# Optimization experiments

Measured on AMD Instinct MI355X. Metric: run time of the kernel, lower is better.

## Reference

```python
import jax, jax.numpy as jnp
import numpy as np

IMPOSSIBLE = -10000.0
TAGSET_SIZE = 64
NUM_TAGS = TAGSET_SIZE + 2  # C = 66
START_IDX = NUM_TAGS - 2
STOP_IDX = NUM_TAGS - 1
B, L, D = 32, 1024, 1024


def setup_inputs() -> dict:
    key = jax.random.key(0)
    k1, k2, k3, k4, k5 = jax.random.split(key, 5)
    features = jax.random.normal(k1, (B, L, D), dtype=jnp.float32)
    ys = jax.random.randint(k2, (B, L), 0, TAGSET_SIZE).astype(jnp.int64)
    masks = jnp.ones((B, L), dtype=jnp.float32)
    fc_w = jax.random.normal(k3, (D, NUM_TAGS), dtype=jnp.float32) / np.sqrt(D)
    fc_b = jax.random.normal(k4, (NUM_TAGS,), dtype=jnp.float32) * 0.01
    transitions = jax.random.normal(k5, (NUM_TAGS, NUM_TAGS), dtype=jnp.float32)
    # transitions TO start and FROM stop are impossible (torch indexing [to, from])
    transitions = transitions.at[START_IDX, :].set(IMPOSSIBLE)
    transitions = transitions.at[:, STOP_IDX].set(IMPOSSIBLE)
    return {"features": features, "ys": ys, "masks": masks,
            "fc_w": fc_w, "fc_b": fc_b, "transitions": transitions}


def _forward_algorithm(feats, masks, transitions):
    """CRF partition function. feats: [B,L,C], masks: [B,L] -> [B]."""
    Bb, Ll, C = feats.shape
    scores0 = jnp.full((Bb, C), IMPOSSIBLE, dtype=feats.dtype).at[:, START_IDX].set(0.0)

    def step(scores, xs):
        emit_t, m_t = xs  # emit_t: [B,C], m_t: [B]
        # score_t[b, j] = logsumexp_i( scores[b,i] + trans[j,i] + emit[b,j] )
        score_t = jax.nn.logsumexp(
            scores[:, None, :] + transitions[None, :, :] + emit_t[:, :, None], axis=-1)
        scores = score_t * m_t[:, None] + scores * (1.0 - m_t[:, None])
        return scores, None

    xs = (jnp.swapaxes(feats, 0, 1), jnp.swapaxes(masks, 0, 1))  # [L,B,C], [L,B]
    scores, _ = jax.lax.scan(step, scores0, xs)
    return jax.nn.logsumexp(scores + transitions[STOP_IDX][None, :], axis=-1)


def _score_sentence(feats, tags, masks, transitions):
    """Score of the gold tag path. feats: [B,L,C], tags: [B,L] -> [B]."""
    Bb, Ll, C = feats.shape
    emit = jnp.take_along_axis(feats, tags[:, :, None], axis=2)[:, :, 0]  # [B,L]
    start = jnp.full((Bb, 1), START_IDX, dtype=tags.dtype)
    tags_ext = jnp.concatenate([start, tags], axis=1)  # [B,L+1]
    trans_sc = transitions[tags_ext[:, 1:], tags_ext[:, :-1]]  # [B,L]
    lengths = masks.sum(1).astype(jnp.int32)  # [B]
    last_tag = tags_ext[jnp.arange(Bb), lengths]  # [B]
    last_score = transitions[STOP_IDX, last_tag]
    return ((trans_sc + emit) * masks).sum(1) + last_score


def reference(features, ys, masks, fc_w, fc_b, transitions):
    feats = jnp.einsum('bld,dc->blc', features, fc_w) + fc_b  # [B,L,C]
    masks_ = masks.astype(feats.dtype)
    forward_score = _forward_algorithm(feats, masks_, transitions)  # [B]
    gold_score = _score_sentence(feats, ys.astype(jnp.int32), masks_, transitions)  # [B]
    return (forward_score, gold_score)
```

## Files before the change

kernel.cpp:

```cpp
#include <hip/hip_runtime.h>
#include <hip/hip_bf16.h>
#include <stdint.h>


#define START_IDX 64
#define STOP_IDX 65
#define LN2F 0.6931471805599453f

typedef __attribute__((ext_vector_type(4))) float f32x4;
typedef __attribute__((ext_vector_type(8))) __bf16 bf16x8;
typedef __attribute__((ext_vector_type(4))) __bf16 bf16x4;

__device__ __forceinline__ void gload_lds16(const void* g, void* l) {
  __builtin_amdgcn_global_load_lds(
      (const __attribute__((address_space(1))) void*)g,
      (__attribute__((address_space(3))) void*)l, 16, 0, 0);
}

template <int CTRL>
__device__ __forceinline__ float dpp_mov(float v) {
  return __int_as_float(
      __builtin_amdgcn_update_dpp(0, __float_as_int(v), CTRL, 0xF, 0xF, true));
}
__device__ __forceinline__ float wave_max64(float v) {
  v = fmaxf(v, dpp_mov<0xB1>(v));
  v = fmaxf(v, dpp_mov<0x4E>(v));
  v = fmaxf(v, dpp_mov<0x141>(v));
  v = fmaxf(v, dpp_mov<0x140>(v));
  v = fmaxf(v, dpp_mov<0x142>(v));
  v = fmaxf(v, dpp_mov<0x143>(v));
  return v;
}
__device__ __forceinline__ float wave_sum64(float v) {
  v += dpp_mov<0xB1>(v);
  v += dpp_mov<0x4E>(v);
  v += dpp_mov<0x141>(v);
  v += dpp_mov<0x140>(v);
  v += dpp_mov<0x142>(v);
  v += dpp_mov<0x143>(v);
  return v;
}

__global__ __launch_bounds__(256) void crf_wcvt(const float* __restrict__ W,
                                                unsigned short* __restrict__ Wbt) {
  __shared__ float tile[64][65];
  const int t = threadIdx.x;
  const int kb = blockIdx.x;
#pragma unroll
  for (int i = 0; i < 16; ++i) {
    const int f = i * 256 + t;
    const int k = f >> 6, n = f & 63;
    tile[k][n] = W[(kb * 64 + k) * 66 + n];
  }
  __syncthreads();
#pragma unroll
  for (int i = 0; i < 16; ++i) {
    const int f = i * 256 + t;
    const int n = f >> 6, k = f & 63;
    union { __bf16 h; unsigned short u; } cv;
    cv.h = (__bf16)tile[k][n];
    Wbt[n * 1024 + kb * 64 + k] = cv.u;
  }
}

__global__ __launch_bounds__(256) void crf_fwd(const float* __restrict__ features,
                                               const unsigned short* __restrict__ Wbt,
                                               const float* __restrict__ bias,
                                               const float* __restrict__ masks,
                                               const float* __restrict__ trans,
                                               float* __restrict__ featsOut,
                                               float* __restrict__ chunkP,
                                               int* __restrict__ chunkExp) {
  __shared__ __align__(16) float As[4096];
  __shared__ __align__(16) unsigned short Bs[4096];
  __shared__ __align__(16) float expE[64][64];
  __shared__ __align__(16) unsigned short T[2][4096];
  __shared__ float wmax[2][4];
  const int tid = threadIdx.x;
  const int w = tid >> 6, lane = tid & 63, g = lane >> 4, q = lane & 15;
  const int c = blockIdx.x, b = blockIdx.y;

  {
    f32x4 z4 = {0.f, 0.f, 0.f, 0.f};
    *(f32x4*)((char*)T[0] + tid * 16) = z4;
    *(f32x4*)((char*)T[0] + 4096 + tid * 16) = z4;
    __syncthreads();
    if (tid < 64) {
      const int off = tid * 128 + ((2 * tid) ^ ((tid & 7) << 4));
      *(unsigned short*)((char*)T[0] + off) = (unsigned short)0x3F80;
    }
    if (tid < 4) wmax[0][tid] = 1.0f;
  }

  {
    const float* Abase = features + ((size_t)b << 20) + ((size_t)(c << 6) << 10);
    f32x4 acc[4];
#pragma unroll
    for (int nt = 0; nt < 4; ++nt) acc[nt] = (f32x4){0.f, 0.f, 0.f, 0.f};

    const int sA = (q & 7) << 4;
    for (int k0 = 0; k0 < 1024; k0 += 64) {
#pragma unroll
      for (int j = 0; j < 4; ++j) {
        const int row = 16 * w + 4 * j + (lane >> 4);
        const int colb = ((lane & 15) * 16) ^ ((row & 7) << 4);
        gload_lds16((const char*)(Abase + (size_t)row * 1024 + k0) + colb,
                    (char*)As + (16 * w + 4 * j) * 256);
      }
#pragma unroll
      for (int j = 0; j < 2; ++j) {
        const int n = 16 * w + 8 * j + (lane >> 3);
        const int colb = ((lane & 7) * 16) ^ ((n & 7) << 4);
        gload_lds16((const char*)(Wbt + (size_t)n * 1024 + k0) + colb,
                    (char*)Bs + (16 * w + 8 * j) * 128);
      }
      __syncthreads();
#pragma unroll
      for (int kk = 0; kk < 64; kk += 32) {
        const char* Ab = (const char*)As + (16 * w + q) * 256;
        float4 alo = *(const float4*)(Ab + ((kk * 4 + 32 * g) ^ sA));
        float4 ahi = *(const float4*)(Ab + ((kk * 4 + 32 * g + 16) ^ sA));
        bf16x8 af;
        af[0] = (__bf16)alo.x; af[1] = (__bf16)alo.y;
        af[2] = (__bf16)alo.z; af[3] = (__bf16)alo.w;
        af[4] = (__bf16)ahi.x; af[5] = (__bf16)ahi.y;
        af[6] = (__bf16)ahi.z; af[7] = (__bf16)ahi.w;
#pragma unroll
        for (int nt = 0; nt < 4; ++nt) {
          const int n = q + 16 * nt;
          bf16x8 bf = *(const bf16x8*)((const char*)Bs + n * 128 +
                                       ((kk * 2 + 16 * g) ^ ((n & 7) << 4)));
          acc[nt] = __builtin_amdgcn_mfma_f32_16x16x32_bf16(af, bf, acc[nt], 0, 0, 0);
        }
      }
      __syncthreads();
    }
    const float bb0 = bias[q + 0], bb1 = bias[q + 16];
    const float bb2 = bias[q + 32], bb3 = bias[q + 48];
#pragma unroll
    for (int r = 0; r < 4; ++r) {
      const int tl = 16 * w + 4 * g + r;
      float* orow = featsOut + (((size_t)(b << 10) + (c << 6) + tl) << 6) + q;
      const float v0 = acc[0][r] + bb0, v1 = acc[1][r] + bb1;
      const float v2 = acc[2][r] + bb2, v3 = acc[3][r] + bb3;
      orow[0] = v0; orow[16] = v1; orow[32] = v2; orow[48] = v3;
      expE[tl][q + 0]  = __expf(v0);
      expE[tl][q + 16] = __expf(v1);
      expE[tl][q + 32] = __expf(v2);
      expE[tl][q + 48] = __expf(v3);
    }
  }

  bf16x8 Ea0, Ea1;
  {
    const int i = 16 * w + q;
    const float* tp0 = trans + i * 66 + 8 * g;
    const float* tp1 = tp0 + 32;
#pragma unroll
    for (int e = 0; e < 8; ++e) {
      Ea0[e] = (__bf16)__expf(tp0[e]);
      Ea1[e] = (__bf16)__expf(tp1[e]);
    }
  }

  float pv[4][4];
#pragma unroll
  for (int nt = 0; nt < 4; ++nt)
#pragma unroll
    for (int r = 0; r < 4; ++r)
      pv[nt][r] = ((16 * w + 4 * g + r) == (q + 16 * nt)) ? 1.f : 0.f;

  const int t0 = (c == 0) ? 1 : (c << 6);
  const int t1 = (c << 6) + 64;
  const float* mb = masks + (b << 10);
  const int tml = t0 + lane;
  const float mkv = mb[tml > 1023 ? 1023 : tml];

  int e_acc = 0;
  int cur = 0;
  __syncthreads();

  for (int t = t0; t < t1; ++t) {
    const int tl = t - (c << 6);
    const float4 ee = *(const float4*)&expE[tl][16 * w + 4 * g];
    const float m =
        __int_as_float(__builtin_amdgcn_readlane(__float_as_int(mkv), t - t0));
    if (m != 0.f) {
      const char* Tb = (const char*)T[cur];
      f32x4 acc[4];
#pragma unroll
      for (int nt = 0; nt < 4; ++nt) {
        const int n = q + 16 * nt;
        const int sw = (n & 7) << 4;
        bf16x8 B0 = *(const bf16x8*)(Tb + n * 128 + ((16 * g) ^ sw));
        bf16x8 B1 = *(const bf16x8*)(Tb + n * 128 + ((64 + 16 * g) ^ sw));
        f32x4 z = {0.f, 0.f, 0.f, 0.f};
        z = __builtin_amdgcn_mfma_f32_16x16x32_bf16(Ea0, B0, z, 0, 0, 0);
        acc[nt] = __builtin_amdgcn_mfma_f32_16x16x32_bf16(Ea1, B1, z, 0, 0, 0);
      }
      const float4 wm = *(const float4*)wmax[cur];
      const float mx = fmaxf(fmaxf(wm.x, wm.y), fmaxf(wm.z, wm.w));
      const int ex = ((__float_as_int(mx) >> 23) & 0xFF) - 127;
      const float sc = __int_as_float((127 - ex) << 23);
      float ce[4];
      ce[0] = ee.x * sc; ce[1] = ee.y * sc; ce[2] = ee.z * sc; ce[3] = ee.w * sc;
      float lm = 0.f;
#pragma unroll
      for (int nt = 0; nt < 4; ++nt) {
#pragma unroll
        for (int r = 0; r < 4; ++r) {
          float val = acc[nt][r] * ce[r];
          if (m != 1.f) val = m * val + (1.f - m) * sc * pv[nt][r];
          pv[nt][r] = val;
          lm = fmaxf(lm, val);
        }
      }
      lm = wave_max64(lm);
      const int nxt = cur ^ 1;
      char* Tw = (char*)T[nxt];
#pragma unroll
      for (int nt = 0; nt < 4; ++nt) {
        bf16x4 o;
        o[0] = (__bf16)pv[nt][0]; o[1] = (__bf16)pv[nt][1];
        o[2] = (__bf16)pv[nt][2]; o[3] = (__bf16)pv[nt][3];
        const int n = q + 16 * nt;
        *(bf16x4*)(Tw + n * 128 + ((32 * w + 8 * g) ^ ((n & 7) << 4))) = o;
      }
      if (lane == 63) wmax[nxt][w] = lm;
      e_acc += ex;
      __syncthreads();
      cur = nxt;
    }
  }

#pragma unroll
  for (int nt = 0; nt < 4; ++nt)
#pragma unroll
    for (int r = 0; r < 4; ++r)
      chunkP[(((size_t)(b * 16 + c)) << 12) + (size_t)(16 * w + 4 * g + r) * 64 +
             q + 16 * nt] = pv[nt][r];
  if (tid == 0) chunkExp[b * 16 + c] = e_acc;
}

__global__ void crf_fin(const float* __restrict__ feats,
                        const int* __restrict__ ys,
                        const float* __restrict__ masks,
                        const float* __restrict__ trans,
                        const float* __restrict__ chunkP,
                        const int* __restrict__ chunkExp,
                        float* __restrict__ out) {
  __shared__ __align__(16) float vb[64];
  const int lane = threadIdx.x;
  const int b = blockIdx.x >> 1;
  if ((blockIdx.x & 1) == 0) {
    float v = __expf(feats[((size_t)b << 16) + lane]) *
              __expf(trans[lane * 66 + START_IDX]);
    int e_acc = 0;
    for (int cc = 0; cc < 16; ++cc) {
      vb[lane] = v;
      __builtin_amdgcn_wave_barrier();
      const float* Pr = chunkP + (((size_t)(b * 16 + cc)) << 12) + (size_t)lane * 64;
      float q0 = 0.f, q1 = 0.f, q2 = 0.f, q3 = 0.f;
#pragma unroll
      for (int j4 = 0; j4 < 16; ++j4) {
        float4 p = *(const float4*)(Pr + 4 * j4);
        float4 x = ((const float4*)vb)[j4];
        q0 = fmaf(p.x, x.x, q0); q1 = fmaf(p.y, x.y, q1);
        q2 = fmaf(p.z, x.z, q2); q3 = fmaf(p.w, x.w, q3);
      }
      const float qq = (q0 + q1) + (q2 + q3);
      float mx = wave_max64(qq);
      mx = __int_as_float(__builtin_amdgcn_readlane(__float_as_int(mx), 63));
      const int ex = ((__float_as_int(mx) >> 23) & 0xFF) - 127;
      v = qq * __int_as_float((127 - ex) << 23);
      e_acc += ex + chunkExp[b * 16 + cc];
      __builtin_amdgcn_wave_barrier();
    }
    const float sum = wave_sum64(v * __expf(trans[STOP_IDX * 66 + lane]));
    const float s =
        __int_as_float(__builtin_amdgcn_readlane(__float_as_int(sum), 63));
    if (lane == 0) out[b] = __logf(s) + (float)e_acc * LN2F;
  } else {
    const float* fb = feats + ((size_t)b << 16);
    const float* mb = masks + (b << 10);
    const int* yb = ys + (b << 10);
    float s = 0.f, cnt = 0.f;
#pragma unroll
    for (int cc = 0; cc < 16; ++cc) {
      const int t = cc * 64 + lane;
      const float m = mb[t];
      const int y = yb[t];
      const int yp = (t == 0) ? START_IDX : yb[t - 1];
      s += (trans[y * 66 + yp] + fb[t * 64 + y]) * m;
      cnt += m;
    }
    float tot = wave_sum64(s);
    float len = wave_sum64(cnt);
    int totb = __builtin_amdgcn_readlane(__float_as_int(tot), 63);
    int lenb = __builtin_amdgcn_readlane(__float_as_int(len), 63);
    if (lane == 0) {
      const int Lr = (int)__int_as_float(lenb);
      const int last = (Lr == 0) ? START_IDX : yb[Lr - 1];
      out[32 + b] = __int_as_float(totb) + trans[STOP_IDX * 66 + last];
    }
  }
}

extern "C" void kernel_launch(void* const* d_in, const int* in_sizes, int n_in,
                              void* d_out, int out_size, void* d_ws, size_t ws_size,
                              hipStream_t stream) {
  const float* features = (const float*)d_in[0];
  const int* ys         = (const int*)d_in[1];
  const float* masks    = (const float*)d_in[2];
  const float* fc_w     = (const float*)d_in[3];
  const float* fc_b     = (const float*)d_in[4];
  const float* trans    = (const float*)d_in[5];
  float* outp = (float*)d_out;

  char* ws = (char*)d_ws;
  float* feats_ws = (float*)ws;
  unsigned short* Wbt = (unsigned short*)(ws + 8388608);
  float* chunkP = (float*)(ws + 8388608 + 131072);
  int* chunkExp = (int*)(ws + 8388608 + 131072 + 8388608);

  crf_wcvt<<<16, 256, 0, stream>>>(fc_w, Wbt);
  dim3 cg(16, 32);
  crf_fwd<<<cg, 256, 0, stream>>>(features, Wbt, fc_b, masks, trans,
                                  feats_ws, chunkP, chunkExp);
  crf_fin<<<64, 64, 0, stream>>>(feats_ws, ys, masks, trans, chunkP, chunkExp, outp);
}
```

Measured before the change: 274.8 us.

## Halve CRF chunk length, double-buffer GEMM loads, and reuse shared memory

Sequence chunks shrink from 64 to 32 timesteps, so each sequence gets 32 chunks and the forward kernel launches twice as many blocks. The serial per-chunk matrix-product recurrence becomes shorter, at the cost of a longer final chain in crf_fin and twice the chunkP workspace. The projection GEMM now double-buffers its global-to-LDS loads with one barrier per k-step, and its waves split the 32x64 tile in a 2x2 layout. Shared memory is unified into one 32KB buffer that is reused for expE and the transfer matrices, which may raise occupancy. The wave max reduction is also moved after the bf16 stores.

```diff
diff --git a/kernel.cpp b/kernel.cpp
--- a/kernel.cpp
+++ b/kernel.cpp
@@ -71,84 +71,99 @@
                                                float* __restrict__ featsOut,
                                                float* __restrict__ chunkP,
                                                int* __restrict__ chunkExp) {
-  __shared__ __align__(16) float As[4096];
-  __shared__ __align__(16) unsigned short Bs[4096];
-  __shared__ __align__(16) float expE[64][64];
-  __shared__ __align__(16) unsigned short T[2][4096];
+  __shared__ __align__(16) char smem[32768];
   __shared__ float wmax[2][4];
   const int tid = threadIdx.x;
   const int w = tid >> 6, lane = tid & 63, g = lane >> 4, q = lane & 15;
   const int c = blockIdx.x, b = blockIdx.y;
+  const int rb = w & 1, cb = w >> 1;
+
+  const float* Abase = features + ((size_t)b << 20) + ((size_t)c << 15);
 
   {
-    f32x4 z4 = {0.f, 0.f, 0.f, 0.f};
-    *(f32x4*)((char*)T[0] + tid * 16) = z4;
-    *(f32x4*)((char*)T[0] + 4096 + tid * 16) = z4;
-    __syncthreads();
-    if (tid < 64) {
-      const int off = tid * 128 + ((2 * tid) ^ ((tid & 7) << 4));
-      *(unsigned short*)((char*)T[0] + off) = (unsigned short)0x3F80;
-    }
-    if (tid < 4) wmax[0][tid] = 1.0f;
-  }
-
-  {
-    const float* Abase = features + ((size_t)b << 20) + ((size_t)(c << 6) << 10);
-    f32x4 acc[4];
-#pragma unroll
-    for (int nt = 0; nt < 4; ++nt) acc[nt] = (f32x4){0.f, 0.f, 0.f, 0.f};
+    const int arow0 = 8 * w + (lane >> 4);
+    const int acolb = ((lane & 15) * 16);
+    const int brow0 = 16 * w + (lane >> 3);
+    const int bcolb = ((lane & 7) * 16);
+
+    f32x4 acc[2];
+    acc[0] = (f32x4){0.f, 0.f, 0.f, 0.f};
+    acc[1] = (f32x4){0.f, 0.f, 0.f, 0.f};
+
+#pragma unroll
+    for (int j = 0; j < 2; ++j) {
+      const int row = arow0 + 4 * j;
+      gload_lds16((const char*)(Abase + (size_t)row * 1024) +
+                      (acolb ^ ((row & 7) << 4)),
+                  smem + (8 * w + 4 * j) * 256);
+      const int n = brow0 + 8 * j;
+      gload_lds16((const char*)(Wbt + (size_t)n * 1024) +
+                      (bcolb ^ ((n & 7) << 4)),
+                  smem + 16384 + (16 * w + 8 * j) * 128);
+    }
 
     const int sA = (q & 7) << 4;
-    for (int k0 = 0; k0 < 1024; k0 += 64) {
-#pragma unroll
-      for (int j = 0; j < 4; ++j) {
-        const int row = 16 * w + 4 * j + (lane >> 4);
-        const int colb = ((lane & 15) * 16) ^ ((row & 7) << 4);
-        gload_lds16((const char*)(Abase + (size_t)row * 1024 + k0) + colb,
-                    (char*)As + (16 * w + 4 * j) * 256);
-      }
-#pragma unroll
-      for (int j = 0; j < 2; ++j) {
-        const int n = 16 * w + 8 * j + (lane >> 3);
-        const int colb = ((lane & 7) * 16) ^ ((n & 7) << 4);
-        gload_lds16((const char*)(Wbt + (size_t)n * 1024 + k0) + colb,
-                    (char*)Bs + (16 * w + 8 * j) * 128);
-      }
+    for (int kt = 0; kt < 16; ++kt) {
+      const int buf = kt & 1;
       __syncthreads();
-#pragma unroll
-      for (int kk = 0; kk < 64; kk += 32) {
-        const char* Ab = (const char*)As + (16 * w + q) * 256;
-        float4 alo = *(const float4*)(Ab + ((kk * 4 + 32 * g) ^ sA));
-        float4 ahi = *(const float4*)(Ab + ((kk * 4 + 32 * g + 16) ^ sA));
+      if (kt < 15) {
+        const int k0 = (kt + 1) * 64;
+#pragma unroll
+        for (int j = 0; j < 2; ++j) {
+          const int row = arow0 + 4 * j;
+          gload_lds16((const char*)(Abase + (size_t)row * 1024 + k0) +
+                          (acolb ^ ((row & 7) << 4)),
+                      smem + (buf ^ 1) * 8192 + (8 * w + 4 * j) * 256);
+          const int n = brow0 + 8 * j;
+          gload_lds16((const char*)(Wbt + (size_t)n * 1024 + k0) +
+                          (bcolb ^ ((n & 7) << 4)),
+                      smem + 16384 + (buf ^ 1) * 8192 + (16 * w + 8 * j) * 128);
+        }
+      }
+      const char* Ab = smem + buf * 8192 + (16 * rb + q) * 256;
+      const char* Bb = smem + 16384 + buf * 8192;
+#pragma unroll
+      for (int kk = 0; kk < 2; ++kk) {
+        float4 alo = *(const float4*)(Ab + ((kk * 128 + 32 * g) ^ sA));
+        float4 ahi = *(const float4*)(Ab + ((kk * 128 + 32 * g + 16) ^ sA));
         bf16x8 af;
         af[0] = (__bf16)alo.x; af[1] = (__bf16)alo.y;
         af[2] = (__bf16)alo.z; af[3] = (__bf16)alo.w;
         af[4] = (__bf16)ahi.x; af[5] = (__bf16)ahi.y;
         af[6] = (__bf16)ahi.z; af[7] = (__bf16)ahi.w;
 #pragma unroll
-        for (int nt = 0; nt < 4; ++nt) {
-          const int n = q + 16 * nt;
-          bf16x8 bf = *(const bf16x8*)((const char*)Bs + n * 128 +
-                                       ((kk * 2 + 16 * g) ^ ((n & 7) << 4)));
+        for (int nt = 0; nt < 2; ++nt) {
+          const int n = q + 16 * (2 * cb + nt);
+          bf16x8 bf = *(const bf16x8*)(Bb + n * 128 +
+                                       ((kk * 64 + 16 * g) ^ ((n & 7) << 4)));
           acc[nt] = __builtin_amdgcn_mfma_f32_16x16x32_bf16(af, bf, acc[nt], 0, 0, 0);
         }
       }
-      __syncthreads();
-    }
-    const float bb0 = bias[q + 0], bb1 = bias[q + 16];
-    const float bb2 = bias[q + 32], bb3 = bias[q + 48];
+    }
+    const float bb0 = bias[q + 32 * cb], bb1 = bias[q + 32 * cb + 16];
+    float (*expE)[64] = (float(*)[64])smem;
 #pragma unroll
     for (int r = 0; r < 4; ++r) {
-      const int tl = 16 * w + 4 * g + r;
-      float* orow = featsOut + (((size_t)(b << 10) + (c << 6) + tl) << 6) + q;
+      const int tl = 16 * rb + 4 * g + r;
+      float* orow = featsOut + (((size_t)(b << 10) + (c << 5) + tl) << 6) +
+                    q + 32 * cb;
       const float v0 = acc[0][r] + bb0, v1 = acc[1][r] + bb1;
-      const float v2 = acc[2][r] + bb2, v3 = acc[3][r] + bb3;
-      orow[0] = v0; orow[16] = v1; orow[32] = v2; orow[48] = v3;
-      expE[tl][q + 0]  = __expf(v0);
-      expE[tl][q + 16] = __expf(v1);
-      expE[tl][q + 32] = __expf(v2);
-      expE[tl][q + 48] = __expf(v3);
-    }
+      orow[0] = v0; orow[16] = v1;
+      expE[tl][q + 32 * cb] = __expf(v0);
+      expE[tl][q + 32 * cb + 16] = __expf(v1);
+    }
+  }
+
+  {
+    char* T0 = smem + 16384;
+    f32x4 z4 = {0.f, 0.f, 0.f, 0.f};
+    *(f32x4*)(T0 + tid * 32) = z4;
+    *(f32x4*)(T0 + tid * 32 + 16) = z4;
+    const int n = tid >> 2, s = tid & 3;
+    const int d = (2 * n) ^ ((n & 7) << 4);
+    if ((d >> 5) == s)
+      *(unsigned short*)(T0 + n * 128 + d) = (unsigned short)0x3F80;
+    if (tid < 4) wmax[0][tid] = 1.0f;
   }
 
   bf16x8 Ea0, Ea1;
@@ -170,23 +185,24 @@
     for (int r = 0; r < 4; ++r)
       pv[nt][r] = ((16 * w + 4 * g + r) == (q + 16 * nt)) ? 1.f : 0.f;
 
-  const int t0 = (c == 0) ? 1 : (c << 6);
-  const int t1 = (c << 6) + 64;
+  const int t0 = (c == 0) ? 1 : (c << 5);
+  const int t1 = (c << 5) + 32;
   const float* mb = masks + (b << 10);
   const int tml = t0 + lane;
   const float mkv = mb[tml > 1023 ? 1023 : tml];
+  float (*expE)[64] = (float(*)[64])smem;
 
   int e_acc = 0;
   int cur = 0;
   __syncthreads();
 
   for (int t = t0; t < t1; ++t) {
-    const int tl = t - (c << 6);
+    const int tl = t - (c << 5);
     const float4 ee = *(const float4*)&expE[tl][16 * w + 4 * g];
     const float m =
         __int_as_float(__builtin_amdgcn_readlane(__float_as_int(mkv), t - t0));
     if (m != 0.f) {
-      const char* Tb = (const char*)T[cur];
+      const char* Tb = smem + 16384 + cur * 8192;
       f32x4 acc[4];
 #pragma unroll
       for (int nt = 0; nt < 4; ++nt) {
@@ -204,7 +220,7 @@
       const float sc = __int_as_float((127 - ex) << 23);
       float ce[4];
       ce[0] = ee.x * sc; ce[1] = ee.y * sc; ce[2] = ee.z * sc; ce[3] = ee.w * sc;
-      float lm = 0.f;
+      float nmax[4];
 #pragma unroll
       for (int nt = 0; nt < 4; ++nt) {
 #pragma unroll
@@ -212,12 +228,12 @@
           float val = acc[nt][r] * ce[r];
           if (m != 1.f) val = m * val + (1.f - m) * sc * pv[nt][r];
           pv[nt][r] = val;
-          lm = fmaxf(lm, val);
         }
-      }
-      lm = wave_max64(lm);
+        nmax[nt] = fmaxf(fmaxf(pv[nt][0], pv[nt][1]),
+                         fmaxf(pv[nt][2], pv[nt][3]));
+      }
       const int nxt = cur ^ 1;
-      char* Tw = (char*)T[nxt];
+      char* Tw = smem + 16384 + nxt * 8192;
 #pragma unroll
       for (int nt = 0; nt < 4; ++nt) {
         bf16x4 o;
@@ -226,6 +242,8 @@
         const int n = q + 16 * nt;
         *(bf16x4*)(Tw + n * 128 + ((32 * w + 8 * g) ^ ((n & 7) << 4))) = o;
       }
+      float lm = wave_max64(fmaxf(fmaxf(nmax[0], nmax[1]),
+                                  fmaxf(nmax[2], nmax[3])));
       if (lane == 63) wmax[nxt][w] = lm;
       e_acc += ex;
       __syncthreads();
@@ -237,9 +255,9 @@
   for (int nt = 0; nt < 4; ++nt)
 #pragma unroll
     for (int r = 0; r < 4; ++r)
-      chunkP[(((size_t)(b * 16 + c)) << 12) + (size_t)(16 * w + 4 * g + r) * 64 +
+      chunkP[(((size_t)(b * 32 + c)) << 12) + (size_t)(16 * w + 4 * g + r) * 64 +
              q + 16 * nt] = pv[nt][r];
-  if (tid == 0) chunkExp[b * 16 + c] = e_acc;
+  if (tid == 0) chunkExp[b * 32 + c] = e_acc;
 }
 
 __global__ void crf_fin(const float* __restrict__ feats,
@@ -256,10 +274,10 @@
     float v = __expf(feats[((size_t)b << 16) + lane]) *
               __expf(trans[lane * 66 + START_IDX]);
     int e_acc = 0;
-    for (int cc = 0; cc < 16; ++cc) {
+    for (int cc = 0; cc < 32; ++cc) {
       vb[lane] = v;
       __builtin_amdgcn_wave_barrier();
-      const float* Pr = chunkP + (((size_t)(b * 16 + cc)) << 12) + (size_t)lane * 64;
+      const float* Pr = chunkP + (((size_t)(b * 32 + cc)) << 12) + (size_t)lane * 64;
       float q0 = 0.f, q1 = 0.f, q2 = 0.f, q3 = 0.f;
 #pragma unroll
       for (int j4 = 0; j4 < 16; ++j4) {
@@ -273,7 +291,7 @@
       mx = __int_as_float(__builtin_amdgcn_readlane(__float_as_int(mx), 63));
       const int ex = ((__float_as_int(mx) >> 23) & 0xFF) - 127;
       v = qq * __int_as_float((127 - ex) << 23);
-      e_acc += ex + chunkExp[b * 16 + cc];
+      e_acc += ex + chunkExp[b * 32 + cc];
       __builtin_amdgcn_wave_barrier();
     }
     const float sum = wave_sum64(v * __expf(trans[STOP_IDX * 66 + lane]));
@@ -321,10 +339,10 @@
   float* feats_ws = (float*)ws;
   unsigned short* Wbt = (unsigned short*)(ws + 8388608);
   float* chunkP = (float*)(ws + 8388608 + 131072);
-  int* chunkExp = (int*)(ws + 8388608 + 131072 + 8388608);
+  int* chunkExp = (int*)(ws + 8388608 + 131072 + 16777216);
 
   crf_wcvt<<<16, 256, 0, stream>>>(fc_w, Wbt);
-  dim3 cg(16, 32);
+  dim3 cg(32, 32);
   crf_fwd<<<cg, 256, 0, stream>>>(features, Wbt, fc_b, masks, trans,
                                   feats_ws, chunkP, chunkExp);
   crf_fin<<<64, 64, 0, stream>>>(feats_ws, ys, masks, trans, chunkP, chunkExp, outp);
```

After: 291.8 us. 6.2% more time.
